# Kernel optimization log

Hardware: AMD Instinct MI355X
Metric: run time of the kernel (lower is better)

## Reference

```python
import jax, jax.numpy as jnp
import numpy as np


def setup_inputs() -> dict:
    key = jax.random.key(0)
    ks = jax.random.split(key, 9)
    B, Lq, Lk, D = 8, 2048, 2048, 768
    s = 1.0 / np.sqrt(D)
    return {
        "queries": jax.random.normal(ks[0], (B, Lq, D), dtype=jnp.float32),
        "values": jax.random.normal(ks[1], (B, Lk, D), dtype=jnp.float32),
        "mask": jax.random.randint(ks[2], (B, Lq, Lk), 0, 2) > 0,
        "Wq": jax.random.normal(ks[3], (D, D), dtype=jnp.float32) * s,
        "bq": jax.random.normal(ks[4], (D,), dtype=jnp.float32) * s,
        "Wk": jax.random.normal(ks[5], (D, D), dtype=jnp.float32) * s,
        "bk": jax.random.normal(ks[6], (D,), dtype=jnp.float32) * s,
        "Wv": jax.random.normal(ks[7], (D, D), dtype=jnp.float32) * s,
        "bv": jax.random.normal(ks[8], (D,), dtype=jnp.float32) * s,
    }


def reference(queries, values, mask, Wq, bq, Wk, bk, Wv, bv):
    NEG = jnp.asarray(-1e9, queries.dtype)
    # torch Linear: x @ W.T + b
    q = jnp.einsum("bld,ed->ble", queries, Wq) + bq
    v = jnp.einsum("bld,ed->ble", values, Wv) + bv
    # NOTE (faithful to source): keys are the key-projection of the
    # already value-projected tensor.
    k = jnp.einsum("bld,ed->ble", v, Wk) + bk
    score = jnp.einsum("bqd,bkd->bqk", q, k)  # [B, Lq, Lk]
    score = jnp.where(mask, score, NEG)
    attn = jax.nn.sigmoid(score)  # sigmoid attention, no normalization
    context = jnp.einsum("bqk,bkd->bqd", attn, v)
    return context
```

## Files before the change

kernel.cpp:

```cpp
#include <hip/hip_runtime.h>
#include <hip/hip_bf16.h>

typedef __bf16 bf16_t;
typedef __bf16 bf16x8 __attribute__((ext_vector_type(8)));
typedef __bf16 bf16x4 __attribute__((ext_vector_type(4)));
typedef float  f32x4  __attribute__((ext_vector_type(4)));

#define LDS_DST(p) ((__attribute__((address_space(3))) void*)(p))
#define GLB_SRC(p) ((const __attribute__((address_space(1))) void*)(p))

#define SBAR()   asm volatile("s_barrier" ::: "memory")
#define WVM8()   asm volatile("s_waitcnt vmcnt(8)" ::: "memory")
#define WVM4()   asm volatile("s_waitcnt vmcnt(4)" ::: "memory")
#define WVM0()   asm volatile("s_waitcnt vmcnt(0)" ::: "memory")
#define SP1()    __builtin_amdgcn_s_setprio(1)
#define SP0()    __builtin_amdgcn_s_setprio(0)

__global__ void __launch_bounds__(256)
convert_kernel(const float* __restrict__ q_in, const float* __restrict__ v_in,
               const float* __restrict__ wq_in, const float* __restrict__ wk_in,
               const float* __restrict__ wv_in,
               bf16_t* __restrict__ qb, bf16_t* __restrict__ vb,
               bf16_t* __restrict__ wqb, bf16_t* __restrict__ wkb,
               bf16_t* __restrict__ wvb) {
  const int tid = threadIdx.x;
  int r = blockIdx.x;
  const float* in; bf16_t* out; int i;
  if (r < 24576) {
    in = (r < 12288) ? q_in : v_in;
    out = (r < 12288) ? qb : vb;
    i = (r % 12288) * 256 + tid;
  } else {
    r -= 24576;
    in = (r < 576) ? wq_in : (r < 1152 ? wk_in : wv_in);
    out = (r < 576) ? wqb : (r < 1152 ? wkb : wvb);
    i = (r % 576) * 256 + tid;
  }
  const float4 v = reinterpret_cast<const float4*>(in)[i];
  bf16x4 o;
  o[0] = (bf16_t)v.x; o[1] = (bf16_t)v.y; o[2] = (bf16_t)v.z; o[3] = (bf16_t)v.w;
  reinterpret_cast<bf16x4*>(out)[i] = o;
}

__global__ void __launch_bounds__(256)
transpose_bf16_kernel(const bf16_t* __restrict__ in, bf16_t* __restrict__ out,
                      int R, int C) {
  __shared__ bf16_t tile[64][72];
  const long base = (long)blockIdx.z * R * C;
  const bf16_t* ib = in + base;
  bf16_t* ob = out + base;
  const int r0 = blockIdx.x * 64, c0 = blockIdx.y * 64;
  const int tid = threadIdx.x;
  const int rr = tid >> 3, cg = tid & 7;
#pragma unroll
  for (int p = 0; p < 2; ++p) {
    int row = p * 32 + rr;
    bf16x8 v = *reinterpret_cast<const bf16x8*>(ib + (long)(r0 + row) * C + c0 + cg * 8);
    *reinterpret_cast<bf16x8*>(&tile[row][cg * 8]) = v;
  }
  __syncthreads();
#pragma unroll
  for (int p = 0; p < 2; ++p) {
    int c = p * 32 + rr;
    bf16x8 v;
#pragma unroll
    for (int i = 0; i < 8; ++i) v[i] = tile[cg * 8 + i][c];
    *reinterpret_cast<bf16x8*>(ob + (long)(c0 + c) * R + r0 + cg * 8) = v;
  }
}


__device__ __forceinline__ void read_A(const char* smem, int off, bf16x8 (&af)[8], int xk0) {
#pragma unroll
  for (int mf = 0; mf < 4; ++mf)
#pragma unroll
    for (int kk = 0; kk < 2; ++kk)
      af[mf * 2 + kk] = *reinterpret_cast<const bf16x8*>(
          smem + off + mf * 2048 + (kk ? (xk0 ^ 64) : xk0));
}

__device__ __forceinline__ void read_B(const char* smem, int off, bf16x8 (&bf_)[4], int xk0) {
#pragma unroll
  for (int nf = 0; nf < 2; ++nf)
#pragma unroll
    for (int kk = 0; kk < 2; ++kk)
      bf_[nf * 2 + kk] = *reinterpret_cast<const bf16x8*>(
          smem + off + nf * 2048 + (kk ? (xk0 ^ 64) : xk0));
}

template <int MH, int NH>
__device__ __forceinline__ void mfma_q(const bf16x8 (&af)[8], const bf16x8 (&bf_)[4],
                                       f32x4 (&acc)[8][4]) {
#pragma unroll
  for (int mf = 0; mf < 4; ++mf)
#pragma unroll
    for (int nf = 0; nf < 2; ++nf)
#pragma unroll
      for (int kk = 0; kk < 2; ++kk)
        acc[MH * 4 + mf][NH * 2 + nf] = __builtin_amdgcn_mfma_f32_16x16x32_bf16(
            af[mf * 2 + kk], bf_[nf * 2 + kk], acc[MH * 4 + mf][NH * 2 + nf], 0, 0, 0);
}

#define STAGE_A(slot, mh, kt) do {                                            \
  _Pragma("unroll") for (int j_ = 0; j_ < 2; ++j_)                            \
    __builtin_amdgcn_global_load_lds(                                         \
        GLB_SRC(pA + (long)(j_ * 128 + (mh) * 64) * K + (kt)),                \
        LDS_DST(smem + (slot) * 65536 + (arow0 + j_ * 128 + (mh) * 64) * 128),\
        16, 0, 0);                                                            \
} while (0)

#define STAGE_B(slot, nh, kt) do {                                            \
  _Pragma("unroll") for (int j_ = 0; j_ < 2; ++j_)                            \
    __builtin_amdgcn_global_load_lds(                                         \
        GLB_SRC(pB + (long)(j_ * 128 + (nh) * 32) * K + (kt)),                \
        LDS_DST(smem + (slot) * 65536 + 32768 +                               \
                (brow0 + j_ * 128 + (nh) * 32) * 128),                        \
        16, 0, 0);                                                            \
} while (0)

template <int MODE>
__global__ void __launch_bounds__(512, 2)
gemm8p_kernel(const bf16_t* __restrict__ A, const bf16_t* __restrict__ B,
              const float* __restrict__ bias, const int* __restrict__ mask,
              void* __restrict__ Cout, int M, int N, int K,
              long sA, long sB, long sC, long sMask,
              const bf16_t* __restrict__ A2, const bf16_t* __restrict__ B2,
              const float* __restrict__ bias2, void* __restrict__ C2) {
  __shared__ __align__(1024) char smem[131072];

  const int gx = gridDim.x, gy = gridDim.y;
  int f0 = blockIdx.x + gx * (blockIdx.y + gy * blockIdx.z);
  const int nwg = gx * gy * (int)gridDim.z;
  const int q8 = nwg >> 3, r8 = nwg & 7;
  const int xcd = f0 & 7, idx = f0 >> 3;
  int f1 = (xcd < r8 ? xcd * (q8 + 1) : r8 * (q8 + 1) + (xcd - r8) * q8) + idx;
  int bxi, byi, bz;
  if constexpr (MODE == 1) {
    bxi = f1 & 7;
    const int byL = (f1 >> 3) & 1;
    const int st = (f1 >> 4) & 3;
    bz = f1 >> 6;
    byi = st * 2 + byL;
  } else {
    byi = f1 % gy;
    const int t = f1 / gy;
    bxi = t % gx;
    bz = t / gx;
  }

  const bf16_t* Ab; const bf16_t* Bb;
  const float* biasp = bias; void* Cp = Cout;
  if constexpr (MODE == 0) {
    if (bz) { Ab = A2; Bb = B2; biasp = bias2; Cp = C2; }
    else    { Ab = A;  Bb = B; }
  } else {
    Ab = A + bz * sA; Bb = B + bz * sB;
  }
  const int bm = bxi * 256, bn = byi * 256;
  const int tid = threadIdx.x;
  const int wave = tid >> 6, lane = tid & 63;
  const int wr = wave >> 2, wc = wave & 3;
  const int l15 = lane & 15, lg = lane >> 4;
  const int xk0 = (lg * 16) ^ ((lane & 7) << 4);
  const int NT = K >> 6;

  const int lr = lane >> 3;
  const int cgs = ((lane & 7) ^ lr) * 8;
  const int arow0 = wave * 8;
  const int brow0 = (wave >> 2) * 64 + (wave & 3) * 8;
  const bf16_t* pA = Ab + (long)(bm + arow0 + lr) * K + cgs;
  const bf16_t* pB = Bb + (long)(bn + brow0 + lr) * K + cgs;

  const int aoff = wr * 16384 + l15 * 128;
  const int boff = 32768 + wc * 8192 + l15 * 128;

  f32x4 acc[8][4] = {};
  bf16x8 afX[8], bfB[4], bf0[4];

  STAGE_A(0, 0, 0); STAGE_B(0, 0, 0); STAGE_B(0, 1, 0); STAGE_A(0, 1, 0);
  STAGE_A(1, 0, 64); STAGE_B(1, 0, 64);
  STAGE_B(1, 1, 64); STAGE_A(1, 1, 64);
  WVM8();
  SBAR();
  read_A(smem, aoff + 0, afX, xk0);
  read_B(smem, boff + 0, bf0, xk0);

  int slot = 0;
  for (int t = 0; t + 2 < NT; ++t) {
    const int so = slot * 65536, sn = (slot ^ 1) * 65536;
    const int k2 = (t + 2) << 6;
    read_B(smem, so + boff + 4096, bfB, xk0);
    STAGE_A(slot, 0, k2); STAGE_B(slot, 0, k2);
    SP1(); mfma_q<0, 0>(afX, bf0, acc); SP0();
    SP1(); mfma_q<0, 1>(afX, bfB, acc); SP0();
    read_A(smem, so + aoff + 8192, afX, xk0);
    WVM8(); SBAR();
    SP1(); mfma_q<1, 1>(afX, bfB, acc); SP0();
    SP1(); mfma_q<1, 0>(afX, bf0, acc); SP0();
    read_A(smem, sn + aoff + 0, afX, xk0);
    read_B(smem, sn + boff + 0, bf0, xk0);
    STAGE_B(slot, 1, k2); STAGE_A(slot, 1, k2);
    WVM8(); SBAR();
    slot ^= 1;
  }

  {
    const int so = slot * 65536, sn = (slot ^ 1) * 65536;
    read_B(smem, so + boff + 4096, bfB, xk0);
    SP1(); mfma_q<0, 0>(afX, bf0, acc); SP0();
    SP1(); mfma_q<0, 1>(afX, bfB, acc); SP0();
    read_A(smem, so + aoff + 8192, afX, xk0);
    WVM4(); SBAR();
    SP1(); mfma_q<1, 1>(afX, bfB, acc); SP0();
    SP1(); mfma_q<1, 0>(afX, bf0, acc); SP0();
    read_A(smem, sn + aoff + 0, afX, xk0);
    read_B(smem, sn + boff + 0, bf0, xk0);
    WVM0(); SBAR();
    read_B(smem, sn + boff + 4096, bfB, xk0);
    SP1(); mfma_q<0, 0>(afX, bf0, acc); SP0();
    SP1(); mfma_q<0, 1>(afX, bfB, acc); SP0();
    read_A(smem, sn + aoff + 8192, afX, xk0);
    SP1(); mfma_q<1, 1>(afX, bfB, acc); SP0();
    SP1(); mfma_q<1, 0>(afX, bf0, acc); SP0();
  }

  float* eb = (float*)smem;
  const int lrow = tid >> 3, t7 = tid & 7;
#pragma unroll
  for (int rd = 0; rd < 4; ++rd) {
    const int growt = rd * 32 + lrow + ((lrow >> 5) * 96);
    const long rowbase = (long)(bm + growt) * N + bn;
    int4 m4[8];
    if constexpr (MODE == 1) {
      const int* mrow = mask + bz * sMask + rowbase;
#pragma unroll
      for (int q = 0; q < 8; ++q)
        m4[q] = *reinterpret_cast<const int4*>(mrow + (q * 8 + t7) * 4);
    }
    __syncthreads();
#pragma unroll
    for (int fi = 0; fi < 2; ++fi)
#pragma unroll
      for (int nf = 0; nf < 4; ++nf)
#pragma unroll
        for (int r = 0; r < 4; ++r) {
          const int lr2 = wr * 32 + fi * 16 + lg * 4 + r;
          eb[lr2 * 256 + wc * 64 + nf * 16 + l15] = acc[rd * 2 + fi][nf][r];
        }
    __syncthreads();
#pragma unroll
    for (int q = 0; q < 8; ++q) {
      const int c4 = (q * 8 + t7) * 4;
      const f32x4 v = *reinterpret_cast<const f32x4*>(&eb[lrow * 256 + c4]);
      if constexpr (MODE == 1) {
        bf16x4 o;
        o[0] = (bf16_t)(m4[q].x ? __builtin_amdgcn_rcpf(1.f + __expf(-v[0])) : 0.f);
        o[1] = (bf16_t)(m4[q].y ? __builtin_amdgcn_rcpf(1.f + __expf(-v[1])) : 0.f);
        o[2] = (bf16_t)(m4[q].z ? __builtin_amdgcn_rcpf(1.f + __expf(-v[2])) : 0.f);
        o[3] = (bf16_t)(m4[q].w ? __builtin_amdgcn_rcpf(1.f + __expf(-v[3])) : 0.f);
        *reinterpret_cast<bf16x4*>((bf16_t*)Cp + bz * sC + rowbase + c4) = o;
      } else if constexpr (MODE == 0) {
        const f32x4 b4 = *reinterpret_cast<const f32x4*>(biasp + bn + c4);
        bf16x4 o;
        o[0] = (bf16_t)(v[0] + b4[0]); o[1] = (bf16_t)(v[1] + b4[1]);
        o[2] = (bf16_t)(v[2] + b4[2]); o[3] = (bf16_t)(v[3] + b4[3]);
        *reinterpret_cast<bf16x4*>((bf16_t*)Cp + bz * sC + rowbase + c4) = o;
      } else {
        *reinterpret_cast<f32x4*>((float*)Cp + bz * sC + rowbase + c4) = v;
      }
    }
  }
}

extern "C" void kernel_launch(void* const* d_in, const int* in_sizes, int n_in,
                              void* d_out, int out_size, void* d_ws, size_t ws_size,
                              hipStream_t stream) {
  const float* queries = (const float*)d_in[0];
  const float* values  = (const float*)d_in[1];
  const int*   mask    = (const int*)d_in[2];
  const float* Wq = (const float*)d_in[3];
  const float* bq = (const float*)d_in[4];
  const float* Wk = (const float*)d_in[5];
  const float* bk = (const float*)d_in[6];
  const float* Wv = (const float*)d_in[7];
  const float* bv = (const float*)d_in[8];

  char* ws = (char*)d_ws;
  bf16_t* qb  = (bf16_t*)(ws + 0);
  bf16_t* vb  = (bf16_t*)(ws + 25165824);
  bf16_t* wqb = (bf16_t*)(ws + 50331648);
  bf16_t* wkb = (bf16_t*)(ws + 51511296);
  bf16_t* wvb = (bf16_t*)(ws + 52690944);
  bf16_t* qp  = (bf16_t*)(ws + 53870592);
  bf16_t* vp  = (bf16_t*)(ws + 79036416);
  bf16_t* kp  = (bf16_t*)(ws + 104202240);
  bf16_t* vpT = (bf16_t*)(ws + 129368064);
  bf16_t* P   = (bf16_t*)(ws + 154533888);

  convert_kernel<<<26304, 256, 0, stream>>>(queries, values, Wq, Wk, Wv,
                                            qb, vb, wqb, wkb, wvb);

  const dim3 blk2(512);

  gemm8p_kernel<0><<<dim3(64, 3, 2), blk2, 0, stream>>>(
      qb, wqb, bq, nullptr, qp, 16384, 768, 768, 0, 0, 0, 0,
      vb, wvb, bv, vp);
  gemm8p_kernel<0><<<dim3(64, 3, 1), blk2, 0, stream>>>(
      vp, wkb, bk, nullptr, kp, 16384, 768, 768, 0, 0, 0, 0,
      vp, wkb, bk, kp);

  transpose_bf16_kernel<<<dim3(32, 12, 8), 256, 0, stream>>>(vp, vpT, 2048, 768);

  gemm8p_kernel<1><<<dim3(8, 8, 8), blk2, 0, stream>>>(
      qp, kp, nullptr, mask, P, 2048, 2048, 768,
      (long)2048 * 768, (long)2048 * 768, (long)2048 * 2048, (long)2048 * 2048,
      nullptr, nullptr, nullptr, nullptr);

  gemm8p_kernel<2><<<dim3(8, 3, 8), blk2, 0, stream>>>(
      P, vpT, nullptr, nullptr, d_out, 2048, 768, 2048,
      (long)2048 * 2048, (long)768 * 2048, (long)2048 * 768, 0,
      nullptr, nullptr, nullptr, nullptr);
}
```

Measured before the change: 259.3 us.

## Double-buffer GEMM epilogue staging and prefetch mask; coarsen convert kernel

```diff
diff --git a/kernel.cpp b/kernel.cpp
--- a/kernel.cpp
+++ b/kernel.cpp
@@ -25,21 +25,25 @@
                bf16_t* __restrict__ wvb) {
   const int tid = threadIdx.x;
   int r = blockIdx.x;
-  const float* in; bf16_t* out; int i;
-  if (r < 24576) {
-    in = (r < 12288) ? q_in : v_in;
-    out = (r < 12288) ? qb : vb;
-    i = (r % 12288) * 256 + tid;
+  const float* in; bf16_t* out; int base;
+  if (r < 6144) {
+    in = (r < 3072) ? q_in : v_in;
+    out = (r < 3072) ? qb : vb;
+    base = (r % 3072) * 1024;
   } else {
-    r -= 24576;
-    in = (r < 576) ? wq_in : (r < 1152 ? wk_in : wv_in);
-    out = (r < 576) ? wqb : (r < 1152 ? wkb : wvb);
-    i = (r % 576) * 256 + tid;
-  }
-  const float4 v = reinterpret_cast<const float4*>(in)[i];
-  bf16x4 o;
-  o[0] = (bf16_t)v.x; o[1] = (bf16_t)v.y; o[2] = (bf16_t)v.z; o[3] = (bf16_t)v.w;
-  reinterpret_cast<bf16x4*>(out)[i] = o;
+    r -= 6144;
+    in = (r < 144) ? wq_in : (r < 288 ? wk_in : wv_in);
+    out = (r < 144) ? wqb : (r < 288 ? wkb : wvb);
+    base = (r % 144) * 1024;
+  }
+#pragma unroll
+  for (int j = 0; j < 4; ++j) {
+    const int i = base + j * 256 + tid;
+    const float4 v = reinterpret_cast<const float4*>(in)[i];
+    bf16x4 o;
+    o[0] = (bf16_t)v.x; o[1] = (bf16_t)v.y; o[2] = (bf16_t)v.z; o[3] = (bf16_t)v.w;
+    reinterpret_cast<bf16x4*>(out)[i] = o;
+  }
 }
 
 __global__ void __launch_bounds__(256)
@@ -116,6 +120,15 @@
         LDS_DST(smem + (slot) * 65536 + 32768 +                               \
                 (brow0 + j_ * 128 + (nh) * 32) * 128),                        \
         16, 0, 0);                                                            \
+} while (0)
+
+#define EWRITE(RD, eb) do {                                                   \
+  _Pragma("unroll") for (int fi = 0; fi < 2; ++fi)                            \
+  _Pragma("unroll") for (int nf = 0; nf < 4; ++nf)                            \
+  _Pragma("unroll") for (int r = 0; r < 4; ++r) {                             \
+    const int lr2 = wr * 32 + fi * 16 + lg * 4 + r;                           \
+    (eb)[lr2 * 256 + wc * 64 + nf * 16 + l15] = acc[(RD) * 2 + fi][nf][r];    \
+  }                                                                           \
 } while (0)
 
 template <int MODE>
@@ -224,40 +237,52 @@
     SP1(); mfma_q<1, 0>(afX, bf0, acc); SP0();
   }
 
-  float* eb = (float*)smem;
+  float* eb0 = (float*)smem;
+  float* eb1 = (float*)(smem + 65536);
   const int lrow = tid >> 3, t7 = tid & 7;
+  const int growt0 = lrow + ((lrow >> 5) * 96);
+  int4 m4a[8], m4b[8];
+  if constexpr (MODE == 1) {
+    const int* mrow = mask + bz * sMask + (long)(bm + growt0) * N + bn;
+#pragma unroll
+    for (int q = 0; q < 8; ++q)
+      m4a[q] = *reinterpret_cast<const int4*>(mrow + (q * 8 + t7) * 4);
+  }
+  EWRITE(0, eb0);
+  __syncthreads();
 #pragma unroll
   for (int rd = 0; rd < 4; ++rd) {
-    const int growt = rd * 32 + lrow + ((lrow >> 5) * 96);
-    const long rowbase = (long)(bm + growt) * N + bn;
-    int4 m4[8];
     if constexpr (MODE == 1) {
-      const int* mrow = mask + bz * sMask + rowbase;
-#pragma unroll
-      for (int q = 0; q < 8; ++q)
-        m4[q] = *reinterpret_cast<const int4*>(mrow + (q * 8 + t7) * 4);
+      if (rd < 3) {
+        const int* mrow =
+            mask + bz * sMask + (long)(bm + (rd + 1) * 32 + growt0) * N + bn;
+        if ((rd & 1) == 0) {
+#pragma unroll
+          for (int q = 0; q < 8; ++q)
+            m4b[q] = *reinterpret_cast<const int4*>(mrow + (q * 8 + t7) * 4);
+        } else {
+#pragma unroll
+          for (int q = 0; q < 8; ++q)
+            m4a[q] = *reinterpret_cast<const int4*>(mrow + (q * 8 + t7) * 4);
+        }
+      }
     }
-    __syncthreads();
-#pragma unroll
-    for (int fi = 0; fi < 2; ++fi)
-#pragma unroll
-      for (int nf = 0; nf < 4; ++nf)
-#pragma unroll
-        for (int r = 0; r < 4; ++r) {
-          const int lr2 = wr * 32 + fi * 16 + lg * 4 + r;
-          eb[lr2 * 256 + wc * 64 + nf * 16 + l15] = acc[rd * 2 + fi][nf][r];
-        }
-    __syncthreads();
+    if (rd < 3) {
+      if ((rd & 1) == 0) { EWRITE(rd + 1, eb1); } else { EWRITE(rd + 1, eb0); }
+    }
+    const float* eb = ((rd & 1) == 0) ? eb0 : eb1;
+    const long rowbase = (long)(bm + rd * 32 + growt0) * N + bn;
 #pragma unroll
     for (int q = 0; q < 8; ++q) {
       const int c4 = (q * 8 + t7) * 4;
       const f32x4 v = *reinterpret_cast<const f32x4*>(&eb[lrow * 256 + c4]);
       if constexpr (MODE == 1) {
+        const int4 mq = ((rd & 1) == 0) ? m4a[q] : m4b[q];
         bf16x4 o;
-        o[0] = (bf16_t)(m4[q].x ? __builtin_amdgcn_rcpf(1.f + __expf(-v[0])) : 0.f);
-        o[1] = (bf16_t)(m4[q].y ? __builtin_amdgcn_rcpf(1.f + __expf(-v[1])) : 0.f);
-        o[2] = (bf16_t)(m4[q].z ? __builtin_amdgcn_rcpf(1.f + __expf(-v[2])) : 0.f);
-        o[3] = (bf16_t)(m4[q].w ? __builtin_amdgcn_rcpf(1.f + __expf(-v[3])) : 0.f);
+        o[0] = (bf16_t)(mq.x ? __builtin_amdgcn_rcpf(1.f + __expf(-v[0])) : 0.f);
+        o[1] = (bf16_t)(mq.y ? __builtin_amdgcn_rcpf(1.f + __expf(-v[1])) : 0.f);
+        o[2] = (bf16_t)(mq.z ? __builtin_amdgcn_rcpf(1.f + __expf(-v[2])) : 0.f);
+        o[3] = (bf16_t)(mq.w ? __builtin_amdgcn_rcpf(1.f + __expf(-v[3])) : 0.f);
         *reinterpret_cast<bf16x4*>((bf16_t*)Cp + bz * sC + rowbase + c4) = o;
       } else if constexpr (MODE == 0) {
         const f32x4 b4 = *reinterpret_cast<const f32x4*>(biasp + bn + c4);
@@ -269,6 +294,7 @@
         *reinterpret_cast<f32x4*>((float*)Cp + bz * sC + rowbase + c4) = v;
       }
     }
+    __syncthreads();
   }
 }
 
@@ -297,8 +323,8 @@
   bf16_t* vpT = (bf16_t*)(ws + 129368064);
   bf16_t* P   = (bf16_t*)(ws + 154533888);
 
-  convert_kernel<<<26304, 256, 0, stream>>>(queries, values, Wq, Wk, Wv,
-                                            qb, vb, wqb, wkb, wvb);
+  convert_kernel<<<6576, 256, 0, stream>>>(queries, values, Wq, Wk, Wv,
+                                           qb, vb, wqb, wkb, wvb);
 
   const dim3 blk2(512);
 
```

Measured after the change: 253.5 us (median of 3 runs). 1.02x faster.

## Shrink GEMM tiles to 128x256 with K=32 stages for higher occupancy

Applied to the files above, without the earlier changes.

```diff
diff --git a/kernel.cpp b/kernel.cpp
--- a/kernel.cpp
+++ b/kernel.cpp
@@ -10,11 +10,13 @@
 #define GLB_SRC(p) ((const __attribute__((address_space(1))) void*)(p))
 
 #define SBAR()   asm volatile("s_barrier" ::: "memory")
-#define WVM8()   asm volatile("s_waitcnt vmcnt(8)" ::: "memory")
-#define WVM4()   asm volatile("s_waitcnt vmcnt(4)" ::: "memory")
+#define WVM3()   asm volatile("s_waitcnt vmcnt(3)" ::: "memory")
+#define WVM1()   asm volatile("s_waitcnt vmcnt(1)" ::: "memory")
 #define WVM0()   asm volatile("s_waitcnt vmcnt(0)" ::: "memory")
 #define SP1()    __builtin_amdgcn_s_setprio(1)
 #define SP0()    __builtin_amdgcn_s_setprio(0)
+
+#define SLOT 24576
 
 __global__ void __launch_bounds__(256)
 convert_kernel(const float* __restrict__ q_in, const float* __restrict__ v_in,
@@ -25,21 +27,25 @@
                bf16_t* __restrict__ wvb) {
   const int tid = threadIdx.x;
   int r = blockIdx.x;
-  const float* in; bf16_t* out; int i;
-  if (r < 24576) {
-    in = (r < 12288) ? q_in : v_in;
-    out = (r < 12288) ? qb : vb;
-    i = (r % 12288) * 256 + tid;
+  const float* in; bf16_t* out; int base;
+  if (r < 6144) {
+    in = (r < 3072) ? q_in : v_in;
+    out = (r < 3072) ? qb : vb;
+    base = (r % 3072) * 1024;
   } else {
-    r -= 24576;
-    in = (r < 576) ? wq_in : (r < 1152 ? wk_in : wv_in);
-    out = (r < 576) ? wqb : (r < 1152 ? wkb : wvb);
-    i = (r % 576) * 256 + tid;
-  }
-  const float4 v = reinterpret_cast<const float4*>(in)[i];
-  bf16x4 o;
-  o[0] = (bf16_t)v.x; o[1] = (bf16_t)v.y; o[2] = (bf16_t)v.z; o[3] = (bf16_t)v.w;
-  reinterpret_cast<bf16x4*>(out)[i] = o;
+    r -= 6144;
+    in = (r < 144) ? wq_in : (r < 288 ? wk_in : wv_in);
+    out = (r < 144) ? wqb : (r < 288 ? wkb : wvb);
+    base = (r % 144) * 1024;
+  }
+#pragma unroll
+  for (int j = 0; j < 4; ++j) {
+    const int i = base + j * 256 + tid;
+    const float4 v = reinterpret_cast<const float4*>(in)[i];
+    bf16x4 o;
+    o[0] = (bf16_t)v.x; o[1] = (bf16_t)v.y; o[2] = (bf16_t)v.z; o[3] = (bf16_t)v.w;
+    reinterpret_cast<bf16x4*>(out)[i] = o;
+  }
 }
 
 __global__ void __launch_bounds__(256)
@@ -70,63 +76,52 @@
 }
 
 
-__device__ __forceinline__ void read_A(const char* smem, int off, bf16x8 (&af)[8], int xk0) {
+__device__ __forceinline__ void read_Af(const char* smem, int s, int aoff,
+                                        bf16x8 (&af)[4]) {
 #pragma unroll
   for (int mf = 0; mf < 4; ++mf)
-#pragma unroll
-    for (int kk = 0; kk < 2; ++kk)
-      af[mf * 2 + kk] = *reinterpret_cast<const bf16x8*>(
-          smem + off + mf * 2048 + (kk ? (xk0 ^ 64) : xk0));
-}
-
-__device__ __forceinline__ void read_B(const char* smem, int off, bf16x8 (&bf_)[4], int xk0) {
+    af[mf] = *reinterpret_cast<const bf16x8*>(smem + s + aoff + mf * 1024);
+}
+
+__device__ __forceinline__ void read_Bf(const char* smem, int s, int boff, int nh,
+                                        bf16x8 (&bf_)[2]) {
 #pragma unroll
   for (int nf = 0; nf < 2; ++nf)
-#pragma unroll
-    for (int kk = 0; kk < 2; ++kk)
-      bf_[nf * 2 + kk] = *reinterpret_cast<const bf16x8*>(
-          smem + off + nf * 2048 + (kk ? (xk0 ^ 64) : xk0));
-}
-
-template <int MH, int NH>
-__device__ __forceinline__ void mfma_q(const bf16x8 (&af)[8], const bf16x8 (&bf_)[4],
-                                       f32x4 (&acc)[8][4]) {
-#pragma unroll
-  for (int mf = 0; mf < 4; ++mf)
+    bf_[nf] = *reinterpret_cast<const bf16x8*>(
+        smem + s + boff + nh * 2048 + nf * 1024);
+}
+
+template <int AH, int NH>
+__device__ __forceinline__ void mfma_q(const bf16x8 (&af)[4], const bf16x8 (&bf_)[2],
+                                       f32x4 (&acc)[4][4]) {
+#pragma unroll
+  for (int fi = 0; fi < 2; ++fi)
 #pragma unroll
     for (int nf = 0; nf < 2; ++nf)
-#pragma unroll
-      for (int kk = 0; kk < 2; ++kk)
-        acc[MH * 4 + mf][NH * 2 + nf] = __builtin_amdgcn_mfma_f32_16x16x32_bf16(
-            af[mf * 2 + kk], bf_[nf * 2 + kk], acc[MH * 4 + mf][NH * 2 + nf], 0, 0, 0);
-}
-
-#define STAGE_A(slot, mh, kt) do {                                            \
+      acc[AH * 2 + fi][NH * 2 + nf] = __builtin_amdgcn_mfma_f32_16x16x32_bf16(
+          af[AH * 2 + fi], bf_[nf], acc[AH * 2 + fi][NH * 2 + nf], 0, 0, 0);
+}
+
+#define STAGE_A(s, kt)                                                        \
+  __builtin_amdgcn_global_load_lds(GLB_SRC(pA + (kt)),                        \
+      LDS_DST(smem + (s) * SLOT + wave * 1024), 16, 0, 0)
+
+#define STAGE_B(s, kt) do {                                                   \
   _Pragma("unroll") for (int j_ = 0; j_ < 2; ++j_)                            \
-    __builtin_amdgcn_global_load_lds(                                         \
-        GLB_SRC(pA + (long)(j_ * 128 + (mh) * 64) * K + (kt)),                \
-        LDS_DST(smem + (slot) * 65536 + (arow0 + j_ * 128 + (mh) * 64) * 128),\
+    __builtin_amdgcn_global_load_lds(GLB_SRC(pB + (long)j_ * 128 * K + (kt)), \
+        LDS_DST(smem + (s) * SLOT + 8192 + j_ * 8192 + wave * 1024),          \
         16, 0, 0);                                                            \
 } while (0)
 
-#define STAGE_B(slot, nh, kt) do {                                            \
-  _Pragma("unroll") for (int j_ = 0; j_ < 2; ++j_)                            \
-    __builtin_amdgcn_global_load_lds(                                         \
-        GLB_SRC(pB + (long)(j_ * 128 + (nh) * 32) * K + (kt)),                \
-        LDS_DST(smem + (slot) * 65536 + 32768 +                               \
-                (brow0 + j_ * 128 + (nh) * 32) * 128),                        \
-        16, 0, 0);                                                            \
-} while (0)
-
 template <int MODE>
-__global__ void __launch_bounds__(512, 2)
+__global__ void __launch_bounds__(512, 4)
 gemm8p_kernel(const bf16_t* __restrict__ A, const bf16_t* __restrict__ B,
               const float* __restrict__ bias, const int* __restrict__ mask,
               void* __restrict__ Cout, int M, int N, int K,
               long sA, long sB, long sC, long sMask,
               const bf16_t* __restrict__ A2, const bf16_t* __restrict__ B2,
               const float* __restrict__ bias2, void* __restrict__ C2) {
-  __shared__ __align__(1024) char smem[131072];
+  __shared__ __align__(1024) char smem[49152];
 
   const int gx = gridDim.x, gy = gridDim.y;
   int f0 = blockIdx.x + gx * (blockIdx.y + gy * blockIdx.z);
@@ -136,16 +131,14 @@
   int f1 = (xcd < r8 ? xcd * (q8 + 1) : r8 * (q8 + 1) + (xcd - r8) * q8) + idx;
   int bxi, byi, bz;
   if constexpr (MODE == 1) {
-    bxi = f1 & 7;
-    const int byL = (f1 >> 3) & 1;
-    const int st = (f1 >> 4) & 3;
-    bz = f1 >> 6;
-    byi = st * 2 + byL;
+    bxi = ((f1 >> 6) & 1) * 8 + (f1 & 7);
+    byi = ((f1 >> 4) & 3) * 2 + ((f1 >> 3) & 1);
+    bz = f1 >> 7;
   } else {
-    byi = f1 % gy;
-    const int t = f1 / gy;
-    bxi = t % gx;
-    bz = t / gx;
+    bxi = f1 % gx;
+    const int t_ = f1 / gx;
+    byi = t_ % gy;
+    bz = t_ / gy;
   }
 
   const bf16_t* Ab; const bf16_t* Bb;
@@ -156,101 +149,89 @@
   } else {
     Ab = A + bz * sA; Bb = B + bz * sB;
   }
-  const int bm = bxi * 256, bn = byi * 256;
+  const int bm = bxi * 128, bn = byi * 256;
   const int tid = threadIdx.x;
   const int wave = tid >> 6, lane = tid & 63;
   const int wr = wave >> 2, wc = wave & 3;
   const int l15 = lane & 15, lg = lane >> 4;
-  const int xk0 = (lg * 16) ^ ((lane & 7) << 4);
-  const int NT = K >> 6;
-
-  const int lr = lane >> 3;
-  const int cgs = ((lane & 7) ^ lr) * 8;
-  const int arow0 = wave * 8;
-  const int brow0 = (wave >> 2) * 64 + (wave & 3) * 8;
-  const bf16_t* pA = Ab + (long)(bm + arow0 + lr) * K + cgs;
-  const bf16_t* pB = Bb + (long)(bn + brow0 + lr) * K + cgs;
-
-  const int aoff = wr * 16384 + l15 * 128;
-  const int boff = 32768 + wc * 8192 + l15 * 128;
-
-  f32x4 acc[8][4] = {};
-  bf16x8 afX[8], bfB[4], bf0[4];
-
-  STAGE_A(0, 0, 0); STAGE_B(0, 0, 0); STAGE_B(0, 1, 0); STAGE_A(0, 1, 0);
-  STAGE_A(1, 0, 64); STAGE_B(1, 0, 64);
-  STAGE_B(1, 1, 64); STAGE_A(1, 1, 64);
-  WVM8();
+  const int NT = K >> 5;
+
+  const int srow = wave * 16 + (lane >> 2);
+  const int cgs = ((lane & 3) ^ ((lane >> 2) & 3)) * 8;
+  const bf16_t* pA = Ab + (long)(bm + srow) * K + cgs;
+  const bf16_t* pB = Bb + (long)(bn + srow) * K + cgs;
+
+  const int xk = ((lg ^ (l15 & 3)) << 4);
+  const int aoff = l15 * 64 + xk + wr * 4096;
+  const int boff = 8192 + wc * 4096 + l15 * 64 + xk;
+
+  f32x4 acc[4][4] = {};
+  bf16x8 af[4], bf0[2], bfB[2];
+
+  STAGE_A(0, 0); STAGE_B(0, 0);
+  STAGE_A(1, 32); STAGE_B(1, 32);
+  WVM3();
   SBAR();
-  read_A(smem, aoff + 0, afX, xk0);
-  read_B(smem, boff + 0, bf0, xk0);
-
-  int slot = 0;
+  read_Af(smem, 0, aoff, af);
+  read_Bf(smem, 0, boff, 0, bf0);
+
   for (int t = 0; t + 2 < NT; ++t) {
-    const int so = slot * 65536, sn = (slot ^ 1) * 65536;
-    const int k2 = (t + 2) << 6;
-    read_B(smem, so + boff + 4096, bfB, xk0);
-    STAGE_A(slot, 0, k2); STAGE_B(slot, 0, k2);
-    SP1(); mfma_q<0, 0>(afX, bf0, acc); SP0();
-    SP1(); mfma_q<0, 1>(afX, bfB, acc); SP0();
-    read_A(smem, so + aoff + 8192, afX, xk0);
-    WVM8(); SBAR();
-    SP1(); mfma_q<1, 1>(afX, bfB, acc); SP0();
-    SP1(); mfma_q<1, 0>(afX, bf0, acc); SP0();
-    read_A(smem, sn + aoff + 0, afX, xk0);
-    read_B(smem, sn + boff + 0, bf0, xk0);
-    STAGE_B(slot, 1, k2); STAGE_A(slot, 1, k2);
-    WVM8(); SBAR();
-    slot ^= 1;
+    const int so = (t & 1) * SLOT, sn = ((t + 1) & 1) * SLOT;
+    const int si = t & 1;
+    const int k2 = (t + 2) << 5;
+    read_Bf(smem, so, boff, 1, bfB);
+    STAGE_A(si, k2);
+    SP1(); mfma_q<0, 0>(af, bf0, acc); mfma_q<0, 1>(af, bfB, acc); SP0();
+    WVM1(); SBAR();
+    SP1(); mfma_q<1, 1>(af, bfB, acc); mfma_q<1, 0>(af, bf0, acc); SP0();
+    read_Af(smem, sn, aoff, af);
+    read_Bf(smem, sn, boff, 0, bf0);
+    STAGE_B(si, k2);
+    SBAR();
   }
 
   {
-    const int so = slot * 65536, sn = (slot ^ 1) * 65536;
-    read_B(smem, so + boff + 4096, bfB, xk0);
-    SP1(); mfma_q<0, 0>(afX, bf0, acc); SP0();
-    SP1(); mfma_q<0, 1>(afX, bfB, acc); SP0();
-    read_A(smem, so + aoff + 8192, afX, xk0);
-    WVM4(); SBAR();
-    SP1(); mfma_q<1, 1>(afX, bfB, acc); SP0();
-    SP1(); mfma_q<1, 0>(afX, bf0, acc); SP0();
-    read_A(smem, sn + aoff + 0, afX, xk0);
-    read_B(smem, sn + boff + 0, bf0, xk0);
+    const int so = ((NT - 2) & 1) * SLOT, sn = ((NT - 1) & 1) * SLOT;
+    read_Bf(smem, so, boff, 1, bfB);
+    SP1(); mfma_q<0, 0>(af, bf0, acc); mfma_q<0, 1>(af, bfB, acc); SP0();
     WVM0(); SBAR();
-    read_B(smem, sn + boff + 4096, bfB, xk0);
-    SP1(); mfma_q<0, 0>(afX, bf0, acc); SP0();
-    SP1(); mfma_q<0, 1>(afX, bfB, acc); SP0();
-    read_A(smem, sn + aoff + 8192, afX, xk0);
-    SP1(); mfma_q<1, 1>(afX, bfB, acc); SP0();
-    SP1(); mfma_q<1, 0>(afX, bf0, acc); SP0();
+    SP1(); mfma_q<1, 1>(af, bfB, acc); mfma_q<1, 0>(af, bf0, acc); SP0();
+    read_Af(smem, sn, aoff, af);
+    read_Bf(smem, sn, boff, 0, bf0);
+    SBAR();
+    read_Bf(smem, sn, boff, 1, bfB);
+    SP1(); mfma_q<0, 0>(af, bf0, acc); mfma_q<0, 1>(af, bfB, acc); SP0();
+    SP1(); mfma_q<1, 1>(af, bfB, acc); mfma_q<1, 0>(af, bf0, acc); SP0();
   }
 
   float* eb = (float*)smem;
-  const int lrow = tid >> 3, t7 = tid & 7;
+  const int lrow = tid >> 4, t15 = tid & 15;
 #pragma unroll
   for (int rd = 0; rd < 4; ++rd) {
-    const int growt = rd * 32 + lrow + ((lrow >> 5) * 96);
-    const long rowbase = (long)(bm + growt) * N + bn;
-    int4 m4[8];
+    const long rowbase = (long)(bm + rd * 32 + lrow) * N + bn;
+    int4 m4[4];
     if constexpr (MODE == 1) {
       const int* mrow = mask + bz * sMask + rowbase;
 #pragma unroll
-      for (int q = 0; q < 8; ++q)
-        m4[q] = *reinterpret_cast<const int4*>(mrow + (q * 8 + t7) * 4);
+      for (int q = 0; q < 4; ++q)
+        m4[q] = *reinterpret_cast<const int4*>(mrow + (q * 16 + t15) * 4);
     }
     __syncthreads();
-#pragma unroll
-    for (int fi = 0; fi < 2; ++fi)
-#pragma unroll
-      for (int nf = 0; nf < 4; ++nf)
-#pragma unroll
-        for (int r = 0; r < 4; ++r) {
-          const int lr2 = wr * 32 + fi * 16 + lg * 4 + r;
-          eb[lr2 * 256 + wc * 64 + nf * 16 + l15] = acc[rd * 2 + fi][nf][r];
-        }
+    if (wr == (rd >> 1)) {
+#pragma unroll
+      for (int fi = 0; fi < 2; ++fi)
+#pragma unroll
+        for (int nf = 0; nf < 4; ++nf)
+#pragma unroll
+          for (int r = 0; r < 4; ++r) {
+            const int rowl = fi * 16 + lg * 4 + r;
+            eb[rowl * 256 + wc * 64 + nf * 16 + l15] = acc[(rd & 1) * 2 + fi][nf][r];
+          }
+    }
     __syncthreads();
 #pragma unroll
-    for (int q = 0; q < 8; ++q) {
-      const int c4 = (q * 8 + t7) * 4;
+    for (int q = 0; q < 4; ++q) {
+      const int c4 = (q * 16 + t15) * 4;
       const f32x4 v = *reinterpret_cast<const f32x4*>(&eb[lrow * 256 + c4]);
       if constexpr (MODE == 1) {
         bf16x4 o;
@@ -297,26 +278,26 @@
   bf16_t* vpT = (bf16_t*)(ws + 129368064);
   bf16_t* P   = (bf16_t*)(ws + 154533888);
 
-  convert_kernel<<<26304, 256, 0, stream>>>(queries, values, Wq, Wk, Wv,
-                                            qb, vb, wqb, wkb, wvb);
+  convert_kernel<<<6576, 256, 0, stream>>>(queries, values, Wq, Wk, Wv,
+                                           qb, vb, wqb, wkb, wvb);
 
   const dim3 blk2(512);
 
-  gemm8p_kernel<0><<<dim3(64, 3, 2), blk2, 0, stream>>>(
+  gemm8p_kernel<0><<<dim3(128, 3, 2), blk2, 0, stream>>>(
       qb, wqb, bq, nullptr, qp, 16384, 768, 768, 0, 0, 0, 0,
       vb, wvb, bv, vp);
-  gemm8p_kernel<0><<<dim3(64, 3, 1), blk2, 0, stream>>>(
+  gemm8p_kernel<0><<<dim3(128, 3, 1), blk2, 0, stream>>>(
       vp, wkb, bk, nullptr, kp, 16384, 768, 768, 0, 0, 0, 0,
       vp, wkb, bk, kp);
 
   transpose_bf16_kernel<<<dim3(32, 12, 8), 256, 0, stream>>>(vp, vpT, 2048, 768);
 
-  gemm8p_kernel<1><<<dim3(8, 8, 8), blk2, 0, stream>>>(
+  gemm8p_kernel<1><<<dim3(16, 8, 8), blk2, 0, stream>>>(
       qp, kp, nullptr, mask, P, 2048, 2048, 768,
       (long)2048 * 768, (long)2048 * 768, (long)2048 * 2048, (long)2048 * 2048,
       nullptr, nullptr, nullptr, nullptr);
 
-  gemm8p_kernel<2><<<dim3(8, 3, 8), blk2, 0, stream>>>(
+  gemm8p_kernel<2><<<dim3(16, 3, 8), blk2, 0, stream>>>(
       P, vpT, nullptr, nullptr, d_out, 2048, 768, 2048,
       (long)2048 * 2048, (long)768 * 2048, (long)2048 * 768, 0,
       nullptr, nullptr, nullptr, nullptr);
```

After: 279.6 us. 7.8% more time.
